# Kernel optimization log

Hardware: AMD Instinct MI355X
Metric: run time of the kernel (lower is better)

## Reference

```python
import jax, jax.numpy as jnp
import numpy as np

D_IN = 1024
D_OUT = 1024
N_HEADS = 16
HEAD_DIM = D_OUT // N_HEADS
B = 2
S = 2048


def setup_inputs() -> dict:
    key = jax.random.key(0)
    ks = jax.random.split(key, 6)
    scale = 0.02
    x = jax.random.normal(ks[0], (B, S, D_IN), dtype=jnp.float32)
    # torch nn.Linear stores weight as [out, in]; y = x @ W.T + b
    Wq = jax.random.normal(ks[1], (D_OUT, D_IN), dtype=jnp.float32) * scale
    Wk = jax.random.normal(ks[2], (D_OUT, D_IN), dtype=jnp.float32) * scale
    Wv = jax.random.normal(ks[3], (D_OUT, D_IN), dtype=jnp.float32) * scale
    Wo = jax.random.normal(ks[4], (D_OUT, D_OUT), dtype=jnp.float32) * scale
    bo = jax.random.normal(ks[5], (D_OUT,), dtype=jnp.float32) * scale
    return {"x": x, "Wq": Wq, "Wk": Wk, "Wv": Wv, "Wo": Wo, "bo": bo}


def reference(x, Wq, Wk, Wv, Wo, bo):
    b, n, _ = x.shape
    # projections (no qkv bias)
    q = jnp.einsum('bnd,ed->bne', x, Wq).reshape(b, n, N_HEADS, HEAD_DIM).transpose(0, 2, 1, 3)
    k = jnp.einsum('bnd,ed->bne', x, Wk).reshape(b, n, N_HEADS, HEAD_DIM).transpose(0, 2, 1, 3)
    v = jnp.einsum('bnd,ed->bne', x, Wv).reshape(b, n, N_HEADS, HEAD_DIM).transpose(0, 2, 1, 3)
    # scores [b, h, s, s]
    scores = jnp.einsum('bhqd,bhkd->bhqk', q, k) / jnp.sqrt(jnp.float32(HEAD_DIM))
    causal = jnp.tril(jnp.ones((n, n), dtype=bool))
    scores = jnp.where(causal, scores, -jnp.inf)
    attn = jax.nn.softmax(scores, axis=-1)  # dropout p=0 -> identity
    ctx = jnp.einsum('bhqk,bhkd->bhqd', attn, v)
    ctx = ctx.transpose(0, 2, 1, 3).reshape(b, n, D_OUT)
    out = jnp.einsum('bnd,ed->bne', ctx, Wo) + bo
    return out
```

## Files before the change

kernel.cpp:

```cpp
#include <hip/hip_runtime.h>

typedef unsigned short u16;
typedef unsigned int u32;
typedef short bf16x8 __attribute__((ext_vector_type(8)));
typedef short bf16x4 __attribute__((ext_vector_type(4)));
typedef float f32x4 __attribute__((ext_vector_type(4)));
typedef u32 u32x2 __attribute__((ext_vector_type(2)));

#define LOG2E 1.4426950408889634f
#define QSCALE (0.125f * LOG2E)

__device__ __forceinline__ u16 f2b(float f) {
  u32 u = __builtin_bit_cast(u32, f);
  u32 r = (u + 0x7FFFu + ((u >> 16) & 1u)) >> 16;
  return (u16)r;
}

__device__ __forceinline__ bf16x8 cvt8(const float* p) {
  const f32x4 a = *(const f32x4*)p;
  const f32x4 b = *(const f32x4*)(p + 4);
  bf16x8 r = { (short)f2b(a[0]), (short)f2b(a[1]), (short)f2b(a[2]),
               (short)f2b(a[3]), (short)f2b(b[0]), (short)f2b(b[1]),
               (short)f2b(b[2]), (short)f2b(b[3]) };
  return r;
}

__device__ __forceinline__ void gl_lds16(const u16* g, u16* l) {
  __builtin_amdgcn_global_load_lds(
      (const __attribute__((address_space(1))) u32*)(const void*)g,
      (__attribute__((address_space(3))) u32*)(void*)l, 16, 0, 0);
}

__global__ __launch_bounds__(256) void convert_qw_kernel(
    const float* __restrict__ x, const float* __restrict__ wq,
    const float* __restrict__ wk, const float* __restrict__ wv,
    u16* __restrict__ xb, u16* __restrict__ wb) {
  const int i = blockIdx.x * 256 + threadIdx.x;
  if (i >= 917504) return;
  const float* src;
  u16* dst;
  size_t off;
  if (i < 524288) {
    src = x; dst = xb; off = (size_t)i * 8;
  } else {
    const int j = i - 524288;
    const int mat = j >> 17, r = j & 131071;
    src = (mat == 0) ? wq : ((mat == 1) ? wk : wv);
    dst = wb + (size_t)mat * 1048576u;
    off = (size_t)r * 8;
  }
  *(bf16x8*)(dst + off) = cvt8(src + off);
}

__global__ __launch_bounds__(256) void convert_wo_kernel(
    const float* __restrict__ wo, u16* __restrict__ wob) {
  const int i = blockIdx.x * 256 + threadIdx.x;
  if (i >= 131072) return;
  const size_t off = (size_t)i * 8;
  *(bf16x8*)(wob + off) = cvt8(wo + off);
}

__device__ __forceinline__ void gemm_core4(const u16* A, const u16* W,
                                           int m0, int n0, int tid,
                                           u16* As, u16* Bs,
                                           f32x4 (&acc)[4][4]) {
  const int lane = tid & 63, wave = tid >> 6;
  const int wr = wave >> 1, wc = wave & 1;
  const int l15 = lane & 15, quad = lane >> 4;

  const int srow = wave * 16 + (lane >> 2);
  const int csrc =
      (((lane & 3) ^ ((lane >> 2) & 3) ^ ((lane >> 4) & 3)) << 3);
  const u16* ga = A + (size_t)(m0 + srow) * 1024 + csrc;
  const u16* gw = W + (size_t)(n0 + srow) * 1024 + csrc;
  const int lo = wave * 16 * 32;

  const int rswz = (l15 & 3) ^ ((l15 >> 2) & 3);
  const int aoff = (wr * 64 + l15) * 32 + ((quad ^ rswz) << 3);
  const int boff = (wc * 64 + l15) * 32 + ((quad ^ rswz) << 3);

  auto stage = [&](int k0, int db) {
    u16* la = As + db * 4096 + lo;
    u16* lb = Bs + db * 4096 + lo;
    gl_lds16(ga + k0, la);
    gl_lds16(ga + k0 + (size_t)64 * 1024, la + 64 * 32);
    gl_lds16(gw + k0, lb);
    gl_lds16(gw + k0 + (size_t)64 * 1024, lb + 64 * 32);
  };

  stage(0, 0);
  stage(32, 1);
  int db = 0, dbn = 2;
  for (int k0 = 0; k0 < 1024; k0 += 32) {
    if (k0 == 992) {
      asm volatile("s_waitcnt vmcnt(0)" ::: "memory");
    } else {
      asm volatile("s_waitcnt vmcnt(4)" ::: "memory");
    }
    __builtin_amdgcn_s_barrier();
    __builtin_amdgcn_sched_barrier(0);
    if (k0 + 64 < 1024) stage(k0 + 64, dbn);
    const u16* ar = As + db * 4096 + aoff;
    const u16* br = Bs + db * 4096 + boff;
    bf16x8 af[4], bfr[4];
#pragma unroll
    for (int i = 0; i < 4; ++i) af[i] = *(const bf16x8*)(ar + i * 16 * 32);
#pragma unroll
    for (int i = 0; i < 4; ++i) bfr[i] = *(const bf16x8*)(br + i * 16 * 32);
#pragma unroll
    for (int mt = 0; mt < 4; ++mt)
#pragma unroll
      for (int nt = 0; nt < 4; ++nt)
        acc[mt][nt] = __builtin_amdgcn_mfma_f32_16x16x32_bf16(
            af[mt], bfr[nt], acc[mt][nt], 0, 0, 0);
    db = (db == 2) ? 0 : db + 1;
    dbn = (dbn == 2) ? 0 : dbn + 1;
  }
}

__global__ __launch_bounds__(256, 3) void gemm_qkv_kernel(
    const u16* __restrict__ xb, const u16* __restrict__ wb,
    u16* __restrict__ qo, u16* __restrict__ ko, u16* __restrict__ vt) {
  __shared__ __align__(16) u16 As[3 * 4096];
  __shared__ __align__(16) u16 Bs[3 * 4096];
  const int tid = threadIdx.x;
  const int m0 = blockIdx.x * 128;
  const int mat = blockIdx.y >> 3;
  const int n0 = (blockIdx.y & 7) * 128;
  const u16* W = wb + (size_t)mat * 1048576u;

  f32x4 acc[4][4] = {};
  gemm_core4(xb, W, m0, n0, tid, As, Bs, acc);

  const int lane = tid & 63, wave = tid >> 6;
  const int wr = wave >> 1, wc = wave & 1;
  const int l15 = lane & 15, quad = lane >> 4;

  __syncthreads();
  u16* T = ((wave < 2) ? As : Bs) + (wave & 1) * 4608;
  const int rr = lane >> 3;
  const int cc = (lane & 7) * 8;

  if (mat < 2) {
    u16* out = (mat == 0) ? qo : ko;
    const float sc = (mat == 0) ? QSCALE : 1.0f;
#pragma unroll
    for (int mt = 0; mt < 4; ++mt)
#pragma unroll
      for (int nt = 0; nt < 4; ++nt)
#pragma unroll
        for (int r = 0; r < 4; ++r)
          T[(mt * 16 + quad * 4 + r) * 72 + nt * 16 + l15] =
              f2b(acc[mt][nt][r] * sc);
    asm volatile("s_waitcnt lgkmcnt(0)" ::: "memory");
    u16* outp = out + (size_t)(m0 + wr * 64) * 1024 + n0 + wc * 64;
#pragma unroll
    for (int i = 0; i < 8; ++i) {
      const int row = i * 8 + rr;
      const bf16x8 v = *(const bf16x8*)&T[row * 72 + cc];
      *(bf16x8*)&outp[(size_t)row * 1024 + cc] = v;
    }
  } else {
    const int b = m0 >> 11;
    const int sblk = (m0 & 2047) + wr * 64;
#pragma unroll
    for (int mt = 0; mt < 4; ++mt)
#pragma unroll
      for (int nt = 0; nt < 4; ++nt) {
        bf16x4 pk = { (short)f2b(acc[mt][nt][0]), (short)f2b(acc[mt][nt][1]),
                      (short)f2b(acc[mt][nt][2]), (short)f2b(acc[mt][nt][3]) };
        *(bf16x4*)&T[(nt * 16 + l15) * 72 + mt * 16 + quad * 4] = pk;
      }
    asm volatile("s_waitcnt lgkmcnt(0)" ::: "memory");
    u16* vtp = vt + (size_t)(b * 1024 + n0 + wc * 64) * 2048 + sblk;
#pragma unroll
    for (int i = 0; i < 8; ++i) {
      const int erow = i * 8 + rr;
      const bf16x8 v = *(const bf16x8*)&T[erow * 72 + cc];
      *(bf16x8*)&vtp[(size_t)erow * 2048 + cc] = v;
    }
  }
}

__global__ __launch_bounds__(256, 2) void gemm_out_kernel(
    const u16* __restrict__ ctx, const u16* __restrict__ wob,
    const float* __restrict__ bo, float* __restrict__ out) {
  __shared__ __align__(16) u16 As[3 * 8192];
  __shared__ __align__(16) u16 Bs[3 * 4096];
  const int tid = threadIdx.x;
  const int m0 = blockIdx.x * 128;
  const int n0 = blockIdx.y * 64;
  const int lane = tid & 63, wave = tid >> 6;
  const int wr = wave >> 1, wc = wave & 1;
  const int l15 = lane & 15, quad = lane >> 4;

  const int srow = tid >> 3;
  const int csrc = (((tid & 7) ^ ((tid >> 3) & 7)) << 3);
  const u16* ga = ctx + (size_t)(m0 + srow) * 1024 + csrc;
  const u16* gw = wob + (size_t)(n0 + srow) * 1024 + csrc;
  const int lo = wave * 512;
  const int swz = l15 & 7;

  auto stage = [&](int k0, int db) {
    u16* la = As + db * 8192 + lo;
    u16* lb = Bs + db * 4096 + lo;
#pragma unroll
    for (int i = 0; i < 4; ++i)
      gl_lds16(ga + (size_t)(i * 32) * 1024 + k0, la + i * 2048);
#pragma unroll
    for (int i = 0; i < 2; ++i)
      gl_lds16(gw + (size_t)(i * 32) * 1024 + k0, lb + i * 2048);
  };

  f32x4 acc[4][2] = {};
  stage(0, 0);
  stage(64, 1);
  int db = 0, dbn = 2;
  for (int k0 = 0; k0 < 1024; k0 += 64) {
    if (k0 == 960) {
      asm volatile("s_waitcnt vmcnt(0)" ::: "memory");
    } else {
      asm volatile("s_waitcnt vmcnt(6)" ::: "memory");
    }
    __builtin_amdgcn_s_barrier();
    __builtin_amdgcn_sched_barrier(0);
    if (k0 + 128 < 1024) stage(k0 + 128, dbn);
    const u16* ab = As + db * 8192;
    const u16* bb = Bs + db * 4096;
    bf16x8 af[4][2], bfr[2][2];
#pragma unroll
    for (int mt = 0; mt < 4; ++mt)
#pragma unroll
      for (int kk = 0; kk < 2; ++kk)
        af[mt][kk] = *(const bf16x8*)(ab + (wr * 64 + mt * 16 + l15) * 64 +
                                      ((((kk << 2) | quad) ^ swz) << 3));
#pragma unroll
    for (int nt = 0; nt < 2; ++nt)
#pragma unroll
      for (int kk = 0; kk < 2; ++kk)
        bfr[nt][kk] = *(const bf16x8*)(bb + (wc * 32 + nt * 16 + l15) * 64 +
                                       ((((kk << 2) | quad) ^ swz) << 3));
#pragma unroll
    for (int kk = 0; kk < 2; ++kk)
#pragma unroll
      for (int mt = 0; mt < 4; ++mt)
#pragma unroll
        for (int nt = 0; nt < 2; ++nt)
          acc[mt][nt] = __builtin_amdgcn_mfma_f32_16x16x32_bf16(
              af[mt][kk], bfr[nt][kk], acc[mt][nt], 0, 0, 0);
    db = (db == 2) ? 0 : db + 1;
    dbn = (dbn == 2) ? 0 : dbn + 1;
  }

#pragma unroll
  for (int nt = 0; nt < 2; ++nt) {
    const int gc = n0 + wc * 32 + nt * 16 + l15;
    const float bv = bo[gc];
#pragma unroll
    for (int mt = 0; mt < 4; ++mt) {
      const int gr = m0 + wr * 64 + mt * 16 + quad * 4;
#pragma unroll
      for (int r = 0; r < 4; ++r)
        out[(size_t)(gr + r) * 1024 + gc] = acc[mt][nt][r] + bv;
    }
  }
}

__global__ __launch_bounds__(256, 4) void flash_kernel(
    const u16* q, const u16* __restrict__ k,
    const u16* __restrict__ vt, u16* ctx) {
  __shared__ __align__(16) u16 Ks[2][4096];
  __shared__ __align__(16) u16 Vs[2][4096];
  __shared__ __align__(16) u16 plds_all[4][1024];

  const int tid = threadIdx.x;
  const int wave = tid >> 6, lane = tid & 63;
  const int l15 = lane & 15, quad = lane >> 4;

  const int g = blockIdx.x;
  const int xcd = g & 7;
  const int s = g >> 3;
  const int bh_local = s >> 5;
  const int c = s & 31;
  const int qv = (bh_local & 1) ? (31 - c) : c;
  const int q0b = qv * 64;
  const int ntiles = qv + 1;
  const int bh = xcd + 8 * bh_local;
  const int b = bh >> 4, h = bh & 15;
  const int m = q0b + wave * 16 + l15;

  const u16* qrow = q + ((size_t)(b * 2048 + m) * 1024 + h * 64);
  const bf16x8 qf0 = *(const bf16x8*)(qrow + quad * 8);
  const bf16x8 qf1 = *(const bf16x8*)(qrow + 32 + quad * 8);

  const int sr = wave * 16 + (lane >> 3);
  const int csrc = (((lane & 7) ^ ((lane >> 3) & 7)) << 3);
  const u16* kg = k + (size_t)(b * 2048) * 1024 + h * 64;
  const u16* vg = vt + (size_t)(b * 1024 + h * 64) * 2048;
  u16* plds = plds_all[wave];
  const int swz = (l15 & 7);

  f32x4 o[4] = {};
  float m_run = -INFINITY, l_lane = 0.0f;

#pragma unroll
  for (int i = 0; i < 2; ++i) {
    const int r = sr + i * 8;
    gl_lds16(kg + (size_t)r * 1024 + csrc, &Ks[0][wave * 1024 + i * 512]);
    gl_lds16(vg + (size_t)r * 2048 + csrc, &Vs[0][wave * 1024 + i * 512]);
  }
  __syncthreads();

  int buf = 0;
  for (int t = 0; t < ntiles; ++t) {
    const int n0 = t * 64;
    if (t + 1 < ntiles) {
      const int n1 = n0 + 64;
      const int nb = buf ^ 1;
#pragma unroll
      for (int i = 0; i < 2; ++i) {
        const int r = sr + i * 8;
        gl_lds16(kg + (size_t)(n1 + r) * 1024 + csrc,
                 &Ks[nb][wave * 1024 + i * 512]);
        gl_lds16(vg + (size_t)r * 2048 + n1 + csrc,
                 &Vs[nb][wave * 1024 + i * 512]);
      }
    }

    f32x4 st[4];
    __builtin_amdgcn_s_setprio(1);
#pragma unroll
    for (int s4 = 0; s4 < 4; ++s4) {
      const u16* kr = &Ks[buf][(s4 * 16 + l15) * 64];
      const bf16x8 kf0 = *(const bf16x8*)(kr + ((quad ^ swz) << 3));
      const bf16x8 kf1 = *(const bf16x8*)(kr + (((4 | quad) ^ swz) << 3));
      f32x4 a = {};
      a = __builtin_amdgcn_mfma_f32_16x16x32_bf16(kf0, qf0, a, 0, 0, 0);
      a = __builtin_amdgcn_mfma_f32_16x16x32_bf16(kf1, qf1, a, 0, 0, 0);
      st[s4] = a;
    }
    __builtin_amdgcn_s_setprio(0);

    float s[16];
#pragma unroll
    for (int s4 = 0; s4 < 4; ++s4)
#pragma unroll
      for (int r = 0; r < 4; ++r) s[s4 * 4 + r] = st[s4][r];
    if (t == ntiles - 1) {
#pragma unroll
      for (int s4 = 0; s4 < 4; ++s4)
#pragma unroll
        for (int r = 0; r < 4; ++r) {
          const int kv = n0 + s4 * 16 + quad * 4 + r;
          if (kv > m) s[s4 * 4 + r] = -INFINITY;
        }
    }
    float t8[8], t4[4];
#pragma unroll
    for (int i = 0; i < 8; ++i) t8[i] = fmaxf(s[i], s[i + 8]);
#pragma unroll
    for (int i = 0; i < 4; ++i) t4[i] = fmaxf(t8[i], t8[i + 4]);
    float mx = fmaxf(fmaxf(t4[0], t4[1]), fmaxf(t4[2], t4[3]));
    mx = fmaxf(mx, __shfl_xor(mx, 16));
    mx = fmaxf(mx, __shfl_xor(mx, 32));

    float mbase;
    if (__all(mx <= m_run + 8.0f)) {
      mbase = m_run;
    } else {
      mbase = fmaxf(m_run, mx);
      const float alpha = exp2f(m_run - mbase);
      l_lane *= alpha;
#pragma unroll
      for (int dt = 0; dt < 4; ++dt) o[dt] *= alpha;
      m_run = mbase;
    }

    float p[16];
#pragma unroll
    for (int i = 0; i < 16; ++i) p[i] = exp2f(s[i] - mbase);
    float u8[8], u4[4];
#pragma unroll
    for (int i = 0; i < 8; ++i) u8[i] = p[i] + p[i + 8];
#pragma unroll
    for (int i = 0; i < 4; ++i) u4[i] = u8[i] + u8[i + 4];
    l_lane += (u4[0] + u4[1]) + (u4[2] + u4[3]);

#pragma unroll
    for (int s4 = 0; s4 < 4; ++s4) {
      u32 c0, c1;
      asm("v_cvt_pk_bf16_f32 %0, %1, %2"
          : "=v"(c0) : "v"(p[s4 * 4 + 0]), "v"(p[s4 * 4 + 1]));
      asm("v_cvt_pk_bf16_f32 %0, %1, %2"
          : "=v"(c1) : "v"(p[s4 * 4 + 2]), "v"(p[s4 * 4 + 3]));
      const int wchunk = ((s4 * 2 + (quad >> 1)) ^ swz) << 3;
      u32x2 w = { c0, c1 };
      *(u32x2*)&plds[l15 * 64 + wchunk + ((quad & 1) << 2)] = w;
    }
    asm volatile("s_waitcnt lgkmcnt(0)" ::: "memory");

    __builtin_amdgcn_s_setprio(1);
#pragma unroll
    for (int ks = 0; ks < 2; ++ks) {
      const bf16x8 pf =
          *(const bf16x8*)&plds[l15 * 64 + (((ks * 4 + quad) ^ swz) << 3)];
#pragma unroll
      for (int dt = 0; dt < 4; ++dt) {
        const u16* vr = &Vs[buf][(dt * 16 + l15) * 64];
        const bf16x8 vf =
            *(const bf16x8*)(vr + ((((ks << 2) | quad) ^ swz) << 3));
        o[dt] = __builtin_amdgcn_mfma_f32_16x16x32_bf16(vf, pf, o[dt], 0, 0, 0);
      }
    }
    __builtin_amdgcn_s_setprio(0);

    __syncthreads();
    buf ^= 1;
  }

  float l = l_lane;
  l += __shfl_xor(l, 16);
  l += __shfl_xor(l, 32);
  const float inv = 1.0f / l;
  u16* crow = ctx + ((size_t)(b * 2048 + m) * 1024 + h * 64);
#pragma unroll
  for (int dt = 0; dt < 4; ++dt) {
    bf16x4 ov = { (short)f2b(o[dt][0] * inv), (short)f2b(o[dt][1] * inv),
                  (short)f2b(o[dt][2] * inv), (short)f2b(o[dt][3] * inv) };
    *(bf16x4*)&crow[dt * 16 + quad * 4] = ov;
  }
}

extern "C" void kernel_launch(void* const* d_in, const int* in_sizes, int n_in,
                              void* d_out, int out_size, void* d_ws,
                              size_t ws_size, hipStream_t stream) {
  const float* x  = (const float*)d_in[0];
  const float* wq = (const float*)d_in[1];
  const float* wk = (const float*)d_in[2];
  const float* wv = (const float*)d_in[3];
  const float* wo = (const float*)d_in[4];
  const float* bo = (const float*)d_in[5];
  float* out = (float*)d_out;

  u16* qb = (u16*)d_ws;
  u16* kb = qb + 4194304u;
  u16* vt = kb + 4194304u;
  u16* ctx = qb;
  u16* wob = kb;

  u16* xb = (u16*)d_out;
  u16* wb = xb + 4194304u;

  convert_qw_kernel<<<3584, 256, 0, stream>>>(x, wq, wk, wv, xb, wb);
  gemm_qkv_kernel<<<dim3(32, 24), 256, 0, stream>>>(xb, wb, qb, kb, vt);
  flash_kernel<<<1024, 256, 0, stream>>>(qb, kb, vt, ctx);
  convert_wo_kernel<<<512, 256, 0, stream>>>(wo, wob);
  gemm_out_kernel<<<dim3(32, 16), 256, 0, stream>>>(ctx, wob, bo, out);
}
```

Before: 180.6 us.

## Enlarge QKV GEMM tile to 256x128 with per-wave 64x128 subtiles

The QKV projection GEMM moves from a 128x128 tile (2x2 waves of 64x64) to a 256x128 tile where each wave computes 64 rows by the full 128 columns. Each A fragment is reused across 8 MFMA column tiles, and the grid shrinks from 768 to 384 blocks. The aim is higher arithmetic intensity and less global/LDS traffic per FLOP. In exchange, each thread holds twice the accumulators and the block uses more LDS, so occupancy drops to 2 blocks per CU. The epilogue now writes output in two passes through the LDS staging buffer.

Result: slower. 189.4 us (+4.8%).

```diff
diff --git a/kernel.cpp b/kernel.cpp
--- a/kernel.cpp
+++ b/kernel.cpp
@@ -60,34 +60,44 @@
   *(bf16x8*)(wob + off) = cvt8(wo + off);
 }
 
-__device__ __forceinline__ void gemm_core4(const u16* A, const u16* W,
-                                           int m0, int n0, int tid,
-                                           u16* As, u16* Bs,
-                                           f32x4 (&acc)[4][4]) {
+__global__ __launch_bounds__(256, 2) void gemm_qkv_kernel(
+    const u16* __restrict__ xb, const u16* __restrict__ wb,
+    u16* __restrict__ qo, u16* __restrict__ ko, u16* __restrict__ vt) {
+  __shared__ __align__(16) u16 As[3 * 8192];
+  __shared__ __align__(16) u16 Bs[3 * 4096];
+  const int tid = threadIdx.x;
+  const int m0 = blockIdx.x * 256;
+  const int panel = blockIdx.y;
+  const int mat = panel >> 3;
+  const int n0 = (panel & 7) * 128;
+  const u16* W = wb + (size_t)mat * 1048576u;
+
   const int lane = tid & 63, wave = tid >> 6;
-  const int wr = wave >> 1, wc = wave & 1;
   const int l15 = lane & 15, quad = lane >> 4;
 
-  const int srow = wave * 16 + (lane >> 2);
+  const int srow = tid >> 2;
   const int csrc =
-      (((lane & 3) ^ ((lane >> 2) & 3) ^ ((lane >> 4) & 3)) << 3);
-  const u16* ga = A + (size_t)(m0 + srow) * 1024 + csrc;
+      (((tid & 3) ^ ((tid >> 2) & 3) ^ ((tid >> 4) & 3)) << 3);
+  const u16* ga = xb + (size_t)(m0 + srow) * 1024 + csrc;
   const u16* gw = W + (size_t)(n0 + srow) * 1024 + csrc;
-  const int lo = wave * 16 * 32;
+  const int lo = wave * 512;
 
   const int rswz = (l15 & 3) ^ ((l15 >> 2) & 3);
-  const int aoff = (wr * 64 + l15) * 32 + ((quad ^ rswz) << 3);
-  const int boff = (wc * 64 + l15) * 32 + ((quad ^ rswz) << 3);
+  const int aoff = (wave * 64 + l15) * 32 + ((quad ^ rswz) << 3);
+  const int boff = l15 * 32 + ((quad ^ rswz) << 3);
 
   auto stage = [&](int k0, int db) {
-    u16* la = As + db * 4096 + lo;
+    u16* la = As + db * 8192 + lo;
     u16* lb = Bs + db * 4096 + lo;
-    gl_lds16(ga + k0, la);
-    gl_lds16(ga + k0 + (size_t)64 * 1024, la + 64 * 32);
-    gl_lds16(gw + k0, lb);
-    gl_lds16(gw + k0 + (size_t)64 * 1024, lb + 64 * 32);
+#pragma unroll
+    for (int i = 0; i < 4; ++i)
+      gl_lds16(ga + (size_t)(i * 64) * 1024 + k0, la + i * 2048);
+#pragma unroll
+    for (int i = 0; i < 2; ++i)
+      gl_lds16(gw + (size_t)(i * 64) * 1024 + k0, lb + i * 2048);
   };
 
+  f32x4 acc[4][8] = {};
   stage(0, 0);
   stage(32, 1);
   int db = 0, dbn = 2;
@@ -95,46 +105,27 @@
     if (k0 == 992) {
       asm volatile("s_waitcnt vmcnt(0)" ::: "memory");
     } else {
-      asm volatile("s_waitcnt vmcnt(4)" ::: "memory");
+      asm volatile("s_waitcnt vmcnt(6)" ::: "memory");
     }
     __builtin_amdgcn_s_barrier();
     __builtin_amdgcn_sched_barrier(0);
     if (k0 + 64 < 1024) stage(k0 + 64, dbn);
-    const u16* ar = As + db * 4096 + aoff;
+    const u16* ar = As + db * 8192 + aoff;
     const u16* br = Bs + db * 4096 + boff;
-    bf16x8 af[4], bfr[4];
-#pragma unroll
-    for (int i = 0; i < 4; ++i) af[i] = *(const bf16x8*)(ar + i * 16 * 32);
-#pragma unroll
-    for (int i = 0; i < 4; ++i) bfr[i] = *(const bf16x8*)(br + i * 16 * 32);
+    bf16x8 af[4], bfr[8];
+#pragma unroll
+    for (int i = 0; i < 4; ++i) af[i] = *(const bf16x8*)(ar + i * 512);
+#pragma unroll
+    for (int i = 0; i < 8; ++i) bfr[i] = *(const bf16x8*)(br + i * 512);
 #pragma unroll
     for (int mt = 0; mt < 4; ++mt)
 #pragma unroll
-      for (int nt = 0; nt < 4; ++nt)
+      for (int nt = 0; nt < 8; ++nt)
         acc[mt][nt] = __builtin_amdgcn_mfma_f32_16x16x32_bf16(
             af[mt], bfr[nt], acc[mt][nt], 0, 0, 0);
     db = (db == 2) ? 0 : db + 1;
     dbn = (dbn == 2) ? 0 : dbn + 1;
   }
-}
-
-__global__ __launch_bounds__(256, 3) void gemm_qkv_kernel(
-    const u16* __restrict__ xb, const u16* __restrict__ wb,
-    u16* __restrict__ qo, u16* __restrict__ ko, u16* __restrict__ vt) {
-  __shared__ __align__(16) u16 As[3 * 4096];
-  __shared__ __align__(16) u16 Bs[3 * 4096];
-  const int tid = threadIdx.x;
-  const int m0 = blockIdx.x * 128;
-  const int mat = blockIdx.y >> 3;
-  const int n0 = (blockIdx.y & 7) * 128;
-  const u16* W = wb + (size_t)mat * 1048576u;
-
-  f32x4 acc[4][4] = {};
-  gemm_core4(xb, W, m0, n0, tid, As, Bs, acc);
-
-  const int lane = tid & 63, wave = tid >> 6;
-  const int wr = wave >> 1, wc = wave & 1;
-  const int l15 = lane & 15, quad = lane >> 4;
 
   __syncthreads();
   u16* T = ((wave < 2) ? As : Bs) + (wave & 1) * 4608;
@@ -145,39 +136,48 @@
     u16* out = (mat == 0) ? qo : ko;
     const float sc = (mat == 0) ? QSCALE : 1.0f;
 #pragma unroll
-    for (int mt = 0; mt < 4; ++mt)
-#pragma unroll
-      for (int nt = 0; nt < 4; ++nt)
-#pragma unroll
-        for (int r = 0; r < 4; ++r)
-          T[(mt * 16 + quad * 4 + r) * 72 + nt * 16 + l15] =
-              f2b(acc[mt][nt][r] * sc);
-    asm volatile("s_waitcnt lgkmcnt(0)" ::: "memory");
-    u16* outp = out + (size_t)(m0 + wr * 64) * 1024 + n0 + wc * 64;
-#pragma unroll
-    for (int i = 0; i < 8; ++i) {
-      const int row = i * 8 + rr;
-      const bf16x8 v = *(const bf16x8*)&T[row * 72 + cc];
-      *(bf16x8*)&outp[(size_t)row * 1024 + cc] = v;
+    for (int pass = 0; pass < 2; ++pass) {
+#pragma unroll
+      for (int mt = 0; mt < 4; ++mt)
+#pragma unroll
+        for (int nt2 = 0; nt2 < 4; ++nt2)
+#pragma unroll
+          for (int r = 0; r < 4; ++r)
+            T[(mt * 16 + quad * 4 + r) * 72 + nt2 * 16 + l15] =
+                f2b(acc[mt][pass * 4 + nt2][r] * sc);
+      asm volatile("s_waitcnt lgkmcnt(0)" ::: "memory");
+      u16* outp = out + (size_t)(m0 + wave * 64) * 1024 + n0 + pass * 64;
+#pragma unroll
+      for (int i = 0; i < 8; ++i) {
+        const int row = i * 8 + rr;
+        const bf16x8 v = *(const bf16x8*)&T[row * 72 + cc];
+        *(bf16x8*)&outp[(size_t)row * 1024 + cc] = v;
+      }
+      asm volatile("s_waitcnt lgkmcnt(0)" ::: "memory");
     }
   } else {
     const int b = m0 >> 11;
-    const int sblk = (m0 & 2047) + wr * 64;
-#pragma unroll
-    for (int mt = 0; mt < 4; ++mt)
-#pragma unroll
-      for (int nt = 0; nt < 4; ++nt) {
-        bf16x4 pk = { (short)f2b(acc[mt][nt][0]), (short)f2b(acc[mt][nt][1]),
-                      (short)f2b(acc[mt][nt][2]), (short)f2b(acc[mt][nt][3]) };
-        *(bf16x4*)&T[(nt * 16 + l15) * 72 + mt * 16 + quad * 4] = pk;
+    const int sblk = (m0 & 2047) + wave * 64;
+#pragma unroll
+    for (int pass = 0; pass < 2; ++pass) {
+#pragma unroll
+      for (int mt = 0; mt < 4; ++mt)
+#pragma unroll
+        for (int nt2 = 0; nt2 < 4; ++nt2) {
+          const f32x4 a = acc[mt][pass * 4 + nt2];
+          bf16x4 pk = { (short)f2b(a[0]), (short)f2b(a[1]),
+                        (short)f2b(a[2]), (short)f2b(a[3]) };
+          *(bf16x4*)&T[(nt2 * 16 + l15) * 72 + mt * 16 + quad * 4] = pk;
+        }
+      asm volatile("s_waitcnt lgkmcnt(0)" ::: "memory");
+      u16* vtp = vt + (size_t)(b * 1024 + n0 + pass * 64) * 2048 + sblk;
+#pragma unroll
+      for (int i = 0; i < 8; ++i) {
+        const int erow = i * 8 + rr;
+        const bf16x8 v = *(const bf16x8*)&T[erow * 72 + cc];
+        *(bf16x8*)&vtp[(size_t)erow * 2048 + cc] = v;
       }
-    asm volatile("s_waitcnt lgkmcnt(0)" ::: "memory");
-    u16* vtp = vt + (size_t)(b * 1024 + n0 + wc * 64) * 2048 + sblk;
-#pragma unroll
-    for (int i = 0; i < 8; ++i) {
-      const int erow = i * 8 + rr;
-      const bf16x8 v = *(const bf16x8*)&T[erow * 72 + cc];
-      *(bf16x8*)&vtp[(size_t)erow * 2048 + cc] = v;
+      asm volatile("s_waitcnt lgkmcnt(0)" ::: "memory");
     }
   }
 }
@@ -452,7 +452,7 @@
   u16* wb = xb + 4194304u;
 
   convert_qw_kernel<<<3584, 256, 0, stream>>>(x, wq, wk, wv, xb, wb);
-  gemm_qkv_kernel<<<dim3(32, 24), 256, 0, stream>>>(xb, wb, qb, kb, vt);
+  gemm_qkv_kernel<<<dim3(16, 24), 256, 0, stream>>>(xb, wb, qb, kb, vt);
   flash_kernel<<<1024, 256, 0, stream>>>(qb, kb, vt, ctx);
   convert_wo_kernel<<<512, 256, 0, stream>>>(wo, wob);
   gemm_out_kernel<<<dim3(32, 16), 256, 0, stream>>>(ctx, wob, bo, out);
```
